# Performance work log

Hardware: AMD Instinct MI355X
Metric: run time of the kernel (lower is better)

## Reference

```python
import jax, jax.numpy as jnp
import numpy as np
import math

D_MODEL = 1024
N_HEADS = 16
D_K = D_MODEL // N_HEADS
NB_FEATURES = max(1, math.ceil(math.log(D_MODEL)))  # 7
D_FF = 4096
BH = 4  # block_size_h
BW = 4  # block_size_w
EPS_LN = 1e-6


def gelu_approx(x):
    c = math.sqrt(2.0 / math.pi)
    return 0.5 * x * (1.0 + jnp.tanh(c * (x + 0.044715 * x * x * x)))


def layer_norm(x, alpha, bias):
    # torch .std() uses ddof=1 (unbiased)
    mean = x.mean(axis=-1, keepdims=True)
    std = jnp.std(x, axis=-1, ddof=1, keepdims=True)
    return alpha * (x - mean) / (std + EPS_LN) + bias


def causal_performer(q_in, k_in, v_in, wq, wk, wv, wo, omega):
    B, Sq, D = q_in.shape
    Sk = k_in.shape[1]
    q = (q_in @ wq.T).reshape(B, Sq, N_HEADS, D_K)
    k = (k_in @ wk.T).reshape(B, Sk, N_HEADS, D_K)
    v = (v_in @ wv.T).reshape(B, Sk, N_HEADS, D_K)
    # exp kernel feature map: exp(-0.5 * (x @ omega^T)^2)
    qp = jnp.exp(-0.5 * jnp.square(q @ omega.T))  # (B,Sq,H,nb)
    kp = jnp.exp(-0.5 * jnp.square(k @ omega.T))  # (B,Sk,H,nb)
    qp = qp / (qp.sum(-1, keepdims=True) + 1e-6)
    kp = kp / (kp.sum(-1, keepdims=True) + 1e-6)
    K_cum = jnp.cumsum(kp, axis=1)                               # (B,Sk,H,nb)
    KV_cum = jnp.cumsum(kp[..., None] * v[..., None, :], axis=1)  # (B,Sk,H,nb,dk)
    key_idx = jnp.clip((jnp.arange(Sq) // BH + 1) * BW - 1, None, Sk - 1)
    K_sel = K_cum[:, key_idx]    # (B,Sq,H,nb)
    KV_sel = KV_cum[:, key_idx]  # (B,Sq,H,nb,dk)
    num = jnp.einsum('bshn,bshnd->bshd', qp, KV_sel)
    den = jnp.einsum('bshn,bshn->bsh', qp, K_sel)[..., None]
    out = (num / (den + 1e-6)).reshape(B, Sq, D)
    return out @ wo.T


def setup_inputs() -> dict:
    key = jax.random.key(0)
    ks = jax.random.split(key, 24)
    s = 0.02
    p = {}
    p['x'] = jax.random.normal(ks[0], (2, 4096, D_MODEL), jnp.float32)
    p['lto'] = jax.random.normal(ks[1], (2, 4096, D_MODEL), jnp.float32)
    for i, nm in enumerate(['wq_s', 'wk_s', 'wv_s', 'wo_s']):
        p[nm] = jax.random.normal(ks[2 + i], (D_MODEL, D_MODEL), jnp.float32) * s
    for i, nm in enumerate(['wq_c', 'wk_c', 'wv_c', 'wo_c']):
        p[nm] = jax.random.normal(ks[6 + i], (D_MODEL, D_MODEL), jnp.float32) * s
    p['omega_s'] = jax.random.normal(ks[10], (NB_FEATURES, D_K), jnp.float32) / math.sqrt(D_K)
    p['omega_c'] = jax.random.normal(ks[11], (NB_FEATURES, D_K), jnp.float32) / math.sqrt(D_K)
    p['w1'] = jax.random.normal(ks[12], (D_FF, D_MODEL), jnp.float32) * s
    p['b1'] = jnp.zeros((D_FF,), jnp.float32)
    p['w2'] = jax.random.normal(ks[13], (D_MODEL, D_FF), jnp.float32) * s
    p['b2'] = jnp.zeros((D_MODEL,), jnp.float32)
    for i in range(3):
        p[f'ln{i}_a'] = jnp.ones((D_MODEL,), jnp.float32)
        p[f'ln{i}_b'] = jnp.zeros((D_MODEL,), jnp.float32)
    return p


def reference(x, lto, wq_s, wk_s, wv_s, wo_s, wq_c, wk_c, wv_c, wo_c,
              omega_s, omega_c, w1, b1, w2, b2,
              ln0_a, ln0_b, ln1_a, ln1_b, ln2_a, ln2_b):
    # residual 0: self-attention on x
    xn = layer_norm(x, ln0_a, ln0_b)
    x = x + causal_performer(xn, xn, xn, wq_s, wk_s, wv_s, wo_s, omega_s)
    # residual 1: cross-attention, queries = normed lto, keys/values = updated x
    ln = layer_norm(lto, ln1_a, ln1_b)
    lto = lto + causal_performer(ln, x, x, wq_c, wk_c, wv_c, wo_c, omega_c)
    # residual 2: feed-forward
    fn = layer_norm(lto, ln2_a, ln2_b)
    ff = gelu_approx(fn @ w1.T + b1) @ w2.T + b2
    return lto + ff
```

## Files before the change

kernel.cpp:

```cpp
#include <hip/hip_runtime.h>
#include <cstdint>
#include <cstddef>

typedef __bf16 bf16;
typedef __bf16 bf16x8 __attribute__((ext_vector_type(8)));
typedef __bf16 bf16x4 __attribute__((ext_vector_type(4)));
typedef float  f32x4  __attribute__((ext_vector_type(4)));

#define NB 7
static constexpr int Bq = 2, Sq = 4096, Dm = 1024, Dff = 4096;
static constexpr int Mrows = Bq * Sq;
static constexpr int NCH = Sq / 4;
static constexpr int CSW = 464;

__device__ __forceinline__ void gload16(const void* g, void* l) {
  __builtin_amdgcn_global_load_lds((__attribute__((address_space(1))) void*)g,
                                   (__attribute__((address_space(3))) void*)l,
                                   16, 0, 0);
}

template <int N> __device__ __forceinline__ void wait_vmcnt() {
  asm volatile("s_waitcnt vmcnt(%0)" :: "n"(N) : "memory");
}
__device__ __forceinline__ void wait_lgkm0() {
  asm volatile("s_waitcnt lgkmcnt(0)" ::: "memory");
}

__device__ __forceinline__ float gelu_f(float x) {
  const float c = 0.79788456080286535588f;
  float z = c * (x + 0.044715f * x * x * x);
  float t = 1.f - 2.f / (__expf(2.f * z) + 1.f);
  return 0.5f * x * (1.f + t);
}

struct CvtA {
  const float* s[10];
  bf16* d[10];
  int start[11];
};
__global__ __launch_bounds__(256) void cvt10(CvtA a) {
  const int i = blockIdx.x * 256 + threadIdx.x;
  int r = 0;
#pragma unroll
  for (int k = 1; k < 10; ++k) r += (i >= a.start[k]);
  const int o = i - a.start[r];
  f32x4 v = *(const f32x4*)&a.s[r][(size_t)o * 4];
  bf16x4 ov;
#pragma unroll
  for (int e = 0; e < 4; ++e) ov[e] = (bf16)v[e];
  *(bf16x4*)&a.d[r][(size_t)o * 4] = ov;
}

__global__ __launch_bounds__(256) void ln_kernel(const float* __restrict__ x,
                                                 const float* __restrict__ alpha,
                                                 const float* __restrict__ beta,
                                                 bf16* __restrict__ out) {
  const int row = blockIdx.x, tid = threadIdx.x;
  const float* xr = x + (size_t)row * Dm;
  f32x4 v = *(const f32x4*)&xr[tid * 4];
  float s  = v[0] + v[1] + v[2] + v[3];
  float s2 = v[0]*v[0] + v[1]*v[1] + v[2]*v[2] + v[3]*v[3];
#pragma unroll
  for (int o = 32; o > 0; o >>= 1) { s += __shfl_xor(s, o); s2 += __shfl_xor(s2, o); }
  __shared__ float red[8];
  const int wid = tid >> 6, lane = tid & 63;
  if (lane == 0) { red[wid] = s; red[wid + 4] = s2; }
  __syncthreads();
  s  = red[0] + red[1] + red[2] + red[3];
  s2 = red[4] + red[5] + red[6] + red[7];
  const float mean = s * (1.f / 1024.f);
  float var = (s2 - s * mean) * (1.f / 1023.f);
  var = fmaxf(var, 0.f);
  const float inv = 1.f / (sqrtf(var) + 1e-6f);
  f32x4 a4 = *(const f32x4*)&alpha[tid * 4];
  f32x4 b4 = *(const f32x4*)&beta[tid * 4];
  bf16x4 o4;
#pragma unroll
  for (int e = 0; e < 4; ++e) o4[e] = (bf16)(a4[e] * (v[e] - mean) * inv + b4[e]);
  *(bf16x4*)&out[(size_t)row * Dm + tid * 4] = o4;
}

template <int MODE>
__global__ __launch_bounds__(256, 2) void gemm128(
    const bf16* __restrict__ A, const bf16* __restrict__ Bw,
    int M, int N, int K,
    const float* __restrict__ bias, const float* __restrict__ res,
    float* __restrict__ outF, bf16* __restrict__ outB) {
  constexpr int BM = 128, BN = 128;
  __shared__ __align__(16) bf16 As[2][BM * 64];
  __shared__ __align__(16) bf16 Bs[2][BN * 64];

  const int tid = threadIdx.x;
  const int lane = tid & 63, wid = tid >> 6;
  const int wm = wid >> 1, wn = wid & 1;

  int bid = blockIdx.x;
  const int nwg = gridDim.x;
  bid = (bid & 7) * (nwg >> 3) + (bid >> 3);
  const int nbx = N / BN;
  const int bm = (bid / nbx) * BM, bn = (bid % nbx) * BN;
  const int NT = K >> 6;

  const int srow = tid >> 3;
  const int scol = ((tid & 7) ^ (srow & 7)) * 8;
  const bf16* Ag = A  + (size_t)(bm + srow) * K + scol;
  const bf16* Bg = Bw + (size_t)(bn + srow) * K + scol;

  f32x4 acc[4][4] = {};
  const int lr = lane & 15, uo = lane >> 4;

  auto stA = [&](int buf, int t) {
#pragma unroll
    for (int c = 0; c < 4; ++c)
      gload16(Ag + ((size_t)(c * 32) * K + (size_t)t * 64),
              (char*)(&As[buf][0]) + c * 4096 + wid * 1024);
  };
  auto stB = [&](int buf, int t) {
#pragma unroll
    for (int c = 0; c < 4; ++c)
      gload16(Bg + ((size_t)(c * 32) * K + (size_t)t * 64),
              (char*)(&Bs[buf][0]) + c * 4096 + wid * 1024);
  };

  stA(0, 0); stB(0, 0);
  stA(1, 1); stB(1, 1);
  wait_vmcnt<8>();
  __builtin_amdgcn_s_barrier();

  bf16x8 a[4][2], b[4][2];

  for (int t = 0; t < NT; ++t) {
    const int cur = t & 1;
    const bf16* Asb = &As[cur][0];
    const bf16* Bsb = &Bs[cur][0];

#pragma unroll
    for (int i = 0; i < 4; ++i)
#pragma unroll
      for (int kh = 0; kh < 2; ++kh) {
        const int r = wm * 64 + i * 16 + lr;
        const int u = (kh * 4 + uo) ^ (lr & 7);
        a[i][kh] = *(const bf16x8*)&Asb[r * 64 + u * 8];
      }
#pragma unroll
    for (int j = 0; j < 4; ++j)
#pragma unroll
      for (int kh = 0; kh < 2; ++kh) {
        const int r = wn * 64 + j * 16 + lr;
        const int u = (kh * 4 + uo) ^ (lr & 7);
        b[j][kh] = *(const bf16x8*)&Bsb[r * 64 + u * 8];
      }
    wait_lgkm0();
    __builtin_amdgcn_sched_barrier(0);
    __builtin_amdgcn_s_barrier();
    __builtin_amdgcn_sched_barrier(0);

    if (t + 2 < NT) { stA(cur, t + 2); stB(cur, t + 2); }
    __builtin_amdgcn_sched_barrier(0);

    __builtin_amdgcn_s_setprio(1);
#pragma unroll
    for (int i = 0; i < 4; ++i)
#pragma unroll
      for (int j = 0; j < 4; ++j) {
        acc[i][j] = __builtin_amdgcn_mfma_f32_16x16x32_bf16(a[i][0], b[j][0], acc[i][j], 0, 0, 0);
        acc[i][j] = __builtin_amdgcn_mfma_f32_16x16x32_bf16(a[i][1], b[j][1], acc[i][j], 0, 0, 0);
      }
    __builtin_amdgcn_s_setprio(0);
    __builtin_amdgcn_sched_barrier(0);

    if (t < NT - 2) wait_vmcnt<8>();
    else            wait_vmcnt<0>();
    __builtin_amdgcn_s_barrier();
    __builtin_amdgcn_sched_barrier(0);
  }

#pragma unroll
  for (int f = 0; f < 4; ++f) {
    const int r0 = bm + wm * 64 + f * 16 + (lane >> 4) * 4;
#pragma unroll
    for (int g = 0; g < 4; ++g) {
      const int c = bn + wn * 64 + g * 16 + (lane & 15);
      float bv = 0.f;
      if (MODE == 3 || MODE == 4) bv = bias[c];
#pragma unroll
      for (int r = 0; r < 4; ++r) {
        const size_t idx = (size_t)(r0 + r) * N + c;
        float v = acc[f][g][r];
        if (MODE == 1 || MODE == 2) v += res[idx];
        if (MODE == 3) v = gelu_f(v + bv);
        if (MODE == 4) v += bv + res[idx];
        if (MODE == 0 || MODE == 1 || MODE == 3) outB[idx] = (bf16)v;
        else outF[idx] = v;
      }
    }
  }
}

__global__ __launch_bounds__(512) void perf_cs(
    const bf16* __restrict__ kmat, const bf16* __restrict__ vmat, int ld,
    const float* __restrict__ omega, float* __restrict__ CS,
    float* __restrict__ segtot) {
  const int tid = threadIdx.x;
  const int bh = blockIdx.y, b = bh >> 4, h = bh & 15;
  const int seg = blockIdx.x;
  const int s0 = seg * 512;
  __shared__ __align__(16) bf16 vs[512][64];
  __shared__ float kps[512][8];
  __shared__ float oms[448];

  {
    const bf16* vb = vmat + ((size_t)(b * Sq + s0)) * ld + h * 64;
#pragma unroll
    for (int p = 0; p < 8; ++p) {
      const int row = p * 64 + (tid >> 3), c16 = (tid & 7) * 8;
      *(uint4*)&vs[row][c16 ^ ((row & 7) * 8)] =
          *(const uint4*)&vb[(size_t)row * ld + c16];
    }
  }
  if (tid < 448) oms[tid] = omega[tid];
  __syncthreads();

  {
    const int row = tid;
    const bf16* kr = kmat + ((size_t)(b * Sq + s0 + row)) * ld + h * 64;
    bf16x8 kv[8];
#pragma unroll
    for (int q = 0; q < 8; ++q) kv[q] = *(const bf16x8*)&kr[q * 8];
    float f[NB];
#pragma unroll
    for (int n = 0; n < NB; ++n) f[n] = 0.f;
#pragma unroll
    for (int d = 0; d < 64; ++d) {
      const float kd = (float)kv[d >> 3][d & 7];
#pragma unroll
      for (int n = 0; n < NB; ++n) f[n] += kd * oms[n * 64 + d];
    }
    float sum = 1e-6f, e[NB];
#pragma unroll
    for (int n = 0; n < NB; ++n) { e[n] = __expf(-0.5f * f[n] * f[n]); sum += e[n]; }
    const float inv = 1.f / sum;
#pragma unroll
    for (int n = 0; n < NB; ++n) kps[row][n] = e[n] * inv;
    kps[row][7] = 0.f;
  }
  __syncthreads();

  if (tid < CSW) {
    const int comp = tid;
    float* outb = CS + ((size_t)bh * NCH + seg * 128) * CSW;
    float r = 0.f;
    if (comp < 8) {
      for (int c = 0; c < 128; ++c) {
        if (comp < 7)
          r += kps[4*c][comp] + kps[4*c+1][comp] + kps[4*c+2][comp] + kps[4*c+3][comp];
        outb[(size_t)c * CSW + comp] = r;
      }
    } else if (comp < 456) {
      const int n = (comp - 8) >> 6, d = (comp - 8) & 63;
      for (int c = 0; c < 128; ++c) {
#pragma unroll
        for (int i = 0; i < 4; ++i) {
          const int row = 4 * c + i;
          r += kps[row][n] * (float)vs[row][d ^ ((row & 7) * 8)];
        }
        outb[(size_t)c * CSW + comp] = r;
      }
    } else {
      for (int c = 0; c < 128; ++c) outb[(size_t)c * CSW + comp] = 0.f;
    }
    segtot[((size_t)bh * 8 + seg) * CSW + comp] = r;
  }
}

__global__ __launch_bounds__(256) void perf_scan2(float* __restrict__ segtot) {
  const int bh = blockIdx.x;
  const int c0 = threadIdx.x;
  float run0 = 0.f, run1 = 0.f;
#pragma unroll
  for (int s = 0; s < 8; ++s) {
    float* st = segtot + ((size_t)bh * 8 + s) * CSW;
    float t0 = st[c0]; st[c0] = run0; run0 += t0;
    if (c0 + 256 < CSW) { float t1 = st[c0 + 256]; st[c0 + 256] = run1; run1 += t1; }
  }
}

__global__ __launch_bounds__(256) void perf_out(
    const bf16* __restrict__ qmat, int ldq, const float* __restrict__ omega,
    const float* __restrict__ CS, const float* __restrict__ segtot,
    bf16* __restrict__ attn) {
  const int tid = threadIdx.x;
  const int bh = blockIdx.y, b = bh >> 4, h = bh & 15;
  const int s0 = blockIdx.x * 128;
  const int cg0 = s0 >> 2;
  const int seg = cg0 >> 7;
  __shared__ __align__(16) float Ps[32 * CSW];
  __shared__ float qps[128][8];
  __shared__ float oms[NB * 64];

  {
    const float* src = CS + ((size_t)bh * NCH + cg0) * CSW;
    const float* off = segtot + ((size_t)bh * 8 + seg) * CSW;
    for (int i = tid; i < 32 * CSW / 4; i += 256) {
      f32x4 a = *(const f32x4*)&src[i * 4];
      f32x4 o = *(const f32x4*)&off[(i % (CSW / 4)) * 4];
      a += o;
      *(f32x4*)&Ps[i * 4] = a;
    }
  }
  if (tid < 224) { oms[tid] = omega[tid]; oms[tid + 224] = omega[tid + 224]; }
  __syncthreads();
  {
    const int p = tid >> 1, half = tid & 1;
    const bf16* qr = qmat + ((size_t)(b * Sq + s0 + p)) * ldq + h * 64 + half * 32;
    bf16x8 qv[4];
#pragma unroll
    for (int q = 0; q < 4; ++q) qv[q] = *(const bf16x8*)&qr[q * 8];
    float f[NB];
#pragma unroll
    for (int n = 0; n < NB; ++n) f[n] = 0.f;
#pragma unroll
    for (int d = 0; d < 32; ++d) {
      float qd = (float)qv[d >> 3][d & 7];
#pragma unroll
      for (int n = 0; n < NB; ++n) f[n] += qd * oms[n * 64 + half * 32 + d];
    }
    float sum = 1e-6f;
    float e[NB];
#pragma unroll
    for (int n = 0; n < NB; ++n) {
      float full = f[n] + __shfl_xor(f[n], 1);
      e[n] = __expf(-0.5f * full * full);
      sum += e[n];
    }
    float inv = 1.f / sum;
    if (half == 0) {
      float den = 1e-6f;
      const float* Pr = &Ps[(p >> 2) * CSW];
#pragma unroll
      for (int n = 0; n < NB; ++n) {
        float qn = e[n] * inv;
        qps[p][n] = qn;
        den += qn * Pr[n];
      }
      qps[p][7] = 1.f / den;
    }
  }
  __syncthreads();
  {
    const int d = tid & 63, w = tid >> 6;
    for (int qq = w; qq < 128; qq += 4) {
      const float* Pr = &Ps[(qq >> 2) * CSW + 8 + d];
      float num = 0.f;
#pragma unroll
      for (int n = 0; n < NB; ++n) num += qps[qq][n] * Pr[n * 64];
      attn[((size_t)(b * Sq + s0 + qq)) * Dm + h * 64 + d] = (bf16)(num * qps[qq][7]);
    }
  }
}

extern "C" void kernel_launch(void* const* d_in, const int* in_sizes, int n_in,
                              void* d_out, int out_size, void* d_ws, size_t ws_size,
                              hipStream_t stream) {
  const float* x    = (const float*)d_in[0];
  const float* lto  = (const float*)d_in[1];
  const float* w_s[4] = {(const float*)d_in[2], (const float*)d_in[3],
                         (const float*)d_in[4], (const float*)d_in[5]};
  const float* w_c[4] = {(const float*)d_in[6], (const float*)d_in[7],
                         (const float*)d_in[8], (const float*)d_in[9]};
  const float* omega_s = (const float*)d_in[10];
  const float* omega_c = (const float*)d_in[11];
  const float* w1 = (const float*)d_in[12];
  const float* b1 = (const float*)d_in[13];
  const float* w2 = (const float*)d_in[14];
  const float* b2 = (const float*)d_in[15];
  const float* ln_a[3] = {(const float*)d_in[16], (const float*)d_in[18], (const float*)d_in[20]};
  const float* ln_b[3] = {(const float*)d_in[17], (const float*)d_in[19], (const float*)d_in[21]};

  char* ws = (char*)d_ws;
  size_t off = 0;
  auto alloc = [&](size_t bytes) -> char* {
    char* p = ws + off;
    off += (bytes + 255) & ~(size_t)255;
    return p;
  };

  const size_t actB = (size_t)Mrows * Dm * sizeof(bf16);
  const size_t MB32 = (size_t)Mrows * 2048 * sizeof(bf16);

  bf16* wqkv = (bf16*)alloc((size_t)3072 * 1024 * 2);
  bf16* wo_sb = (bf16*)alloc((size_t)1024 * 1024 * 2);
  bf16* wq_cb = (bf16*)alloc((size_t)1024 * 1024 * 2);
  bf16* wkv  = (bf16*)alloc((size_t)2048 * 1024 * 2);
  bf16* wo_cb = (bf16*)alloc((size_t)1024 * 1024 * 2);
  bf16* w1b = (bf16*)alloc((size_t)Dff * Dm * 2);
  bf16* w2b = (bf16*)alloc((size_t)Dff * Dm * 2);
  bf16* xnb  = (bf16*)alloc(actB);
  char* pool = alloc((size_t)Mrows * Dff * 2);
  bf16* qkvb = (bf16*)pool;
  bf16* kvb  = (bf16*)pool;
  bf16* qb   = (bf16*)(pool + MB32);
  bf16* hb   = (bf16*)pool;
  bf16* attnb= (bf16*)alloc(actB);
  bf16* x2b  = (bf16*)alloc(actB);
  bf16* ln1b = (bf16*)alloc(actB);
  float* lto2 = (float*)alloc((size_t)Mrows * Dm * 4);
  float* CSb  = (float*)alloc((size_t)32 * NCH * CSW * 4);
  float* stb  = (float*)alloc((size_t)32 * 8 * CSW * 4);
  bf16* fnb = xnb;

  {
    CvtA a;
    const float* srcs[10] = {w_s[0], w_s[1], w_s[2], w_s[3], w_c[0],
                             w_c[1], w_c[2], w_c[3], w1, w2};
    bf16* dsts[10] = {wqkv, wqkv + 1048576, wqkv + 2097152, wo_sb, wq_cb,
                      wkv, wkv + 1048576, wo_cb, w1b, w2b};
    const int SM = 262144, LG = 1048576;
    int st = 0;
    for (int i = 0; i < 10; ++i) {
      a.s[i] = srcs[i]; a.d[i] = dsts[i]; a.start[i] = st;
      st += (i < 8) ? SM : LG;
    }
    a.start[10] = st;
    cvt10<<<st / 256, 256, 0, stream>>>(a);
  }

  dim3 gperf(Sq / 128, Bq * 16);
  dim3 gseg(8, Bq * 16);
  const int gQKV = (Mrows / 128) * (3072 / 128);
  const int gKV  = (Mrows / 128) * (2048 / 128);
  const int gFF1 = (Mrows / 128) * (4096 / 128);
  const int gN1k = (Mrows / 128) * (1024 / 128);

  ln_kernel<<<Mrows, 256, 0, stream>>>(x, ln_a[0], ln_b[0], xnb);
  gemm128<0><<<gQKV, 256, 0, stream>>>(xnb, wqkv, Mrows, 3072, 1024, nullptr, nullptr, nullptr, qkvb);
  perf_cs<<<gseg, 512, 0, stream>>>(qkvb + 1024, qkvb + 2048, 3072, omega_s, CSb, stb);
  perf_scan2<<<32, 256, 0, stream>>>(stb);
  perf_out<<<gperf, 256, 0, stream>>>(qkvb, 3072, omega_s, CSb, stb, attnb);
  gemm128<1><<<gN1k, 256, 0, stream>>>(attnb, wo_sb, Mrows, 1024, 1024, nullptr, x, nullptr, x2b);

  ln_kernel<<<Mrows, 256, 0, stream>>>(lto, ln_a[1], ln_b[1], ln1b);
  gemm128<0><<<gN1k, 256, 0, stream>>>(ln1b, wq_cb, Mrows, 1024, 1024, nullptr, nullptr, nullptr, qb);
  gemm128<0><<<gKV, 256, 0, stream>>>(x2b, wkv, Mrows, 2048, 1024, nullptr, nullptr, nullptr, kvb);
  perf_cs<<<gseg, 512, 0, stream>>>(kvb, kvb + 1024, 2048, omega_c, CSb, stb);
  perf_scan2<<<32, 256, 0, stream>>>(stb);
  perf_out<<<gperf, 256, 0, stream>>>(qb, 1024, omega_c, CSb, stb, attnb);
  gemm128<2><<<gN1k, 256, 0, stream>>>(attnb, wo_cb, Mrows, 1024, 1024, nullptr, lto, lto2, nullptr);

  ln_kernel<<<Mrows, 256, 0, stream>>>(lto2, ln_a[2], ln_b[2], fnb);
  gemm128<3><<<gFF1, 256, 0, stream>>>(fnb, w1b, Mrows, 4096, 1024, b1, nullptr, nullptr, hb);
  gemm128<4><<<gN1k, 256, 0, stream>>>(hb, w2b, Mrows, 1024, 4096, b2, lto2, (float*)d_out, nullptr);
}
```

Before: 533.2 us.

## Add 256x256-tile 8-wave GEMM for wide-N projections and FF1

Introduces a new gemm256 kernel with 256x256 output tiles, 512 threads, XOR-swizzled LDS, and interleaved half-tile prefetch with explicit barriers and scheduling fences. It is used for the QKV, KV and FF1 GEMMs, which have large N. The larger tile is meant to raise arithmetic intensity and cut global and LDS traffic per FLOP. In exchange the grid is smaller, which can hurt wave balance, and register and LDS pressure per workgroup is higher.

```diff
diff --git a/kernel.cpp b/kernel.cpp
--- a/kernel.cpp
+++ b/kernel.cpp
@@ -24,6 +24,11 @@
 }
 __device__ __forceinline__ void wait_lgkm0() {
   asm volatile("s_waitcnt lgkmcnt(0)" ::: "memory");
+}
+__device__ __forceinline__ void sbar() {
+  __builtin_amdgcn_sched_barrier(0);
+  __builtin_amdgcn_s_barrier();
+  __builtin_amdgcn_sched_barrier(0);
 }
 
 __device__ __forceinline__ float gelu_f(float x) {
@@ -78,6 +83,154 @@
 #pragma unroll
   for (int e = 0; e < 4; ++e) o4[e] = (bf16)(a4[e] * (v[e] - mean) * inv + b4[e]);
   *(bf16x4*)&out[(size_t)row * Dm + tid * 4] = o4;
+}
+
+template <int MODE>
+__global__ __launch_bounds__(512, 2) void gemm256(
+    const bf16* __restrict__ A, const bf16* __restrict__ Bw,
+    int M, int N, int K,
+    const float* __restrict__ bias, bf16* __restrict__ outB) {
+  __shared__ __align__(16) bf16 As[2][256 * 64];
+  __shared__ __align__(16) bf16 Bs[2][256 * 64];
+
+  const int tid = threadIdx.x;
+  const int lane = tid & 63, wid = tid >> 6;
+  const int wm = wid >> 2, wn = wid & 3;
+
+  int bid = blockIdx.x;
+  const int nwg = gridDim.x;
+  bid = (bid & 7) * (nwg >> 3) + (bid >> 3);
+  const int nbx = N >> 8;
+  const int bm = (bid / nbx) * 256, bn = (bid % nbx) * 256;
+  const int NT = K >> 6, NI = NT >> 1;
+
+  const int srow = tid >> 3;
+  const int scol = ((tid & 7) ^ (srow & 7)) * 8;
+  const bf16* Ag = A  + (size_t)(bm + srow) * K + scol;
+  const bf16* Bg = Bw + (size_t)(bn + srow) * K + scol;
+
+  auto stA = [&](int buf, int H, int t) {
+#pragma unroll
+    for (int c = 0; c < 2; ++c)
+      gload16(Ag + (size_t)(H * 128 + c * 64) * K + (size_t)t * 64,
+              (char*)(&As[buf][0]) + H * 16384 + c * 8192 + wid * 1024);
+  };
+  auto stB = [&](int buf, int H, int t) {
+#pragma unroll
+    for (int c = 0; c < 2; ++c)
+      gload16(Bg + (size_t)(H * 128 + c * 64) * K + (size_t)t * 64,
+              (char*)(&Bs[buf][0]) + H * 16384 + c * 8192 + wid * 1024);
+  };
+
+  f32x4 acc[8][4] = {};
+  const int lr = lane & 15, uo = lane >> 4;
+
+  auto ldA = [&](const bf16* Asb, int mh, bf16x8 (&a)[4][2]) {
+#pragma unroll
+    for (int i = 0; i < 4; ++i)
+#pragma unroll
+      for (int kh = 0; kh < 2; ++kh) {
+        const int r = wm * 128 + mh * 64 + i * 16 + lr;
+        const int u = (kh * 4 + uo) ^ (lr & 7);
+        a[i][kh] = *(const bf16x8*)&Asb[r * 64 + u * 8];
+      }
+  };
+  auto ldB = [&](const bf16* Bsb, int nh, bf16x8 (&b)[2][2]) {
+#pragma unroll
+    for (int j = 0; j < 2; ++j)
+#pragma unroll
+      for (int kh = 0; kh < 2; ++kh) {
+        const int r = wn * 64 + nh * 32 + j * 16 + lr;
+        const int u = (kh * 4 + uo) ^ (lr & 7);
+        b[j][kh] = *(const bf16x8*)&Bsb[r * 64 + u * 8];
+      }
+  };
+  auto mm = [&](int mh, int nh, bf16x8 (&a)[4][2], bf16x8 (&b)[2][2]) {
+    __builtin_amdgcn_s_setprio(1);
+#pragma unroll
+    for (int i = 0; i < 4; ++i)
+#pragma unroll
+      for (int j = 0; j < 2; ++j) {
+        acc[mh*4+i][nh*2+j] = __builtin_amdgcn_mfma_f32_16x16x32_bf16(
+            a[i][0], b[j][0], acc[mh*4+i][nh*2+j], 0, 0, 0);
+        acc[mh*4+i][nh*2+j] = __builtin_amdgcn_mfma_f32_16x16x32_bf16(
+            a[i][1], b[j][1], acc[mh*4+i][nh*2+j], 0, 0, 0);
+      }
+    __builtin_amdgcn_s_setprio(0);
+  };
+
+  stB(0, 0, 0); stB(0, 1, 0); stA(0, 0, 0); stA(0, 1, 0);
+  stB(1, 0, 1); stA(1, 0, 1);
+  wait_vmcnt<4>();
+  __builtin_amdgcn_s_barrier();
+
+  for (int t = 0; t < NI; ++t) {
+    const int u = 2 * t;
+    const bool more = (t + 1 < NI);
+#pragma unroll
+    for (int hf = 0; hf < 2; ++hf) {
+      const bf16* Asb = &As[hf][0];
+      const bf16* Bsb = &Bs[hf][0];
+      bf16x8 a[4][2], b0[2][2], b1[2][2];
+
+      ldA(Asb, 0, a); ldB(Bsb, 0, b0);
+      __builtin_amdgcn_sched_barrier(0);
+      if (hf == 0) stB(1, 1, u + 1);
+      else if (more) stB(0, 1, u + 2);
+      sbar();
+      wait_lgkm0();
+      __builtin_amdgcn_sched_barrier(0);
+      mm(0, 0, a, b0);
+      sbar();
+
+      ldB(Bsb, 1, b1);
+      __builtin_amdgcn_sched_barrier(0);
+      if (hf == 0) stA(1, 1, u + 1);
+      else if (more) stA(0, 1, u + 2);
+      sbar();
+      wait_lgkm0();
+      __builtin_amdgcn_sched_barrier(0);
+      mm(0, 1, a, b1);
+      sbar();
+
+      ldA(Asb, 1, a);
+      __builtin_amdgcn_sched_barrier(0);
+      if (more) { if (hf == 0) stB(0, 0, u + 2); else stB(1, 0, u + 3); }
+      sbar();
+      wait_lgkm0();
+      __builtin_amdgcn_sched_barrier(0);
+      mm(1, 1, a, b1);
+      sbar();
+
+      if (more) { if (hf == 0) stA(0, 0, u + 2); else stA(1, 0, u + 3); }
+      __builtin_amdgcn_sched_barrier(0);
+      sbar();
+      mm(1, 0, a, b0);
+      __builtin_amdgcn_sched_barrier(0);
+      if (hf == 0) { if (more) wait_vmcnt<4>(); else wait_vmcnt<0>(); }
+      else if (more) wait_vmcnt<4>();
+      __builtin_amdgcn_s_barrier();
+      __builtin_amdgcn_sched_barrier(0);
+    }
+  }
+
+#pragma unroll
+  for (int f = 0; f < 8; ++f) {
+    const int r0 = bm + wm * 128 + f * 16 + (lane >> 4) * 4;
+#pragma unroll
+    for (int g = 0; g < 4; ++g) {
+      const int c = bn + wn * 64 + g * 16 + (lane & 15);
+      float bv = 0.f;
+      if (MODE == 3) bv = bias[c];
+#pragma unroll
+      for (int r = 0; r < 4; ++r) {
+        const size_t idx = (size_t)(r0 + r) * N + c;
+        float v = acc[f][g][r];
+        if (MODE == 3) v = gelu_f(v + bv);
+        outB[idx] = (bf16)v;
+      }
+    }
+  }
 }
 
 template <int MODE>
@@ -427,13 +580,13 @@
 
   dim3 gperf(Sq / 128, Bq * 16);
   dim3 gseg(8, Bq * 16);
-  const int gQKV = (Mrows / 128) * (3072 / 128);
-  const int gKV  = (Mrows / 128) * (2048 / 128);
-  const int gFF1 = (Mrows / 128) * (4096 / 128);
+  const int gQKV = (Mrows / 256) * (3072 / 256);
+  const int gKV  = (Mrows / 256) * (2048 / 256);
+  const int gFF1 = (Mrows / 256) * (4096 / 256);
   const int gN1k = (Mrows / 128) * (1024 / 128);
 
   ln_kernel<<<Mrows, 256, 0, stream>>>(x, ln_a[0], ln_b[0], xnb);
-  gemm128<0><<<gQKV, 256, 0, stream>>>(xnb, wqkv, Mrows, 3072, 1024, nullptr, nullptr, nullptr, qkvb);
+  gemm256<0><<<gQKV, 512, 0, stream>>>(xnb, wqkv, Mrows, 3072, 1024, nullptr, qkvb);
   perf_cs<<<gseg, 512, 0, stream>>>(qkvb + 1024, qkvb + 2048, 3072, omega_s, CSb, stb);
   perf_scan2<<<32, 256, 0, stream>>>(stb);
   perf_out<<<gperf, 256, 0, stream>>>(qkvb, 3072, omega_s, CSb, stb, attnb);
@@ -441,13 +594,13 @@
 
   ln_kernel<<<Mrows, 256, 0, stream>>>(lto, ln_a[1], ln_b[1], ln1b);
   gemm128<0><<<gN1k, 256, 0, stream>>>(ln1b, wq_cb, Mrows, 1024, 1024, nullptr, nullptr, nullptr, qb);
-  gemm128<0><<<gKV, 256, 0, stream>>>(x2b, wkv, Mrows, 2048, 1024, nullptr, nullptr, nullptr, kvb);
+  gemm256<0><<<gKV, 512, 0, stream>>>(x2b, wkv, Mrows, 2048, 1024, nullptr, kvb);
   perf_cs<<<gseg, 512, 0, stream>>>(kvb, kvb + 1024, 2048, omega_c, CSb, stb);
   perf_scan2<<<32, 256, 0, stream>>>(stb);
   perf_out<<<gperf, 256, 0, stream>>>(qb, 1024, omega_c, CSb, stb, attnb);
   gemm128<2><<<gN1k, 256, 0, stream>>>(attnb, wo_cb, Mrows, 1024, 1024, nullptr, lto, lto2, nullptr);
 
   ln_kernel<<<Mrows, 256, 0, stream>>>(lto2, ln_a[2], ln_b[2], fnb);
-  gemm128<3><<<gFF1, 256, 0, stream>>>(fnb, w1b, Mrows, 4096, 1024, b1, nullptr, nullptr, hb);
+  gemm256<3><<<gFF1, 512, 0, stream>>>(fnb, w1b, Mrows, 4096, 1024, b1, hb);
   gemm128<4><<<gN1k, 256, 0, stream>>>(hb, w2b, Mrows, 1024, 4096, b2, lto2, (float*)d_out, nullptr);
 }
```

Measured after the change: 531.9 us. Within noise of the previous version (-0.2%).
